# Performance work log

Hardware: AMD Instinct MI355X
Metric: run time of the kernel (lower is better)

The kernel has to match this reference:

```python
import jax, jax.numpy as jnp
import numpy as np

NUM_CODES = 1024
CODE_DIM = 64
EMA_DECAY = 0.99
COMMIT_W = 0.25
EPS = 1e-5
B = 262144


def setup_inputs() -> dict:
    key = jax.random.key(0)
    k1, k2, k3, k4 = jax.random.split(key, 4)
    z = jax.random.normal(k1, (B, CODE_DIM), dtype=jnp.float32)
    weight = jax.random.normal(k2, (NUM_CODES, CODE_DIM), dtype=jnp.float32)
    ema_cluster_size = jax.random.uniform(k3, (NUM_CODES,), dtype=jnp.float32)
    ema_embed_sum = jax.random.normal(k4, (NUM_CODES, CODE_DIM), dtype=jnp.float32)
    return {"z": z, "weight": weight, "ema_cluster_size": ema_cluster_size,
            "ema_embed_sum": ema_embed_sum}


def reference(z, weight, ema_cluster_size, ema_embed_sum):
    # Squared Euclidean distances (argmin equivalent to cdist argmin)
    # d2[b,k] = ||z_b||^2 - 2 z_b . w_k + ||w_k||^2
    z2 = jnp.sum(z * z, axis=-1, keepdims=True)          # (B, 1)
    w2 = jnp.sum(weight * weight, axis=-1)               # (K,)
    d2 = z2 - 2.0 * (z @ weight.T) + w2[None, :]         # (B, K)
    indices = jnp.argmin(d2, axis=-1)                    # (B,)
    z_q = weight[indices]                                # gather with OLD weights

    # EMA codebook update (training, ema_update=True)
    ones = jnp.ones((z.shape[0],), dtype=z.dtype)
    cluster_size = jax.ops.segment_sum(ones, indices, num_segments=NUM_CODES)
    embed_sum = jax.ops.segment_sum(z, indices, num_segments=NUM_CODES)
    new_cs = EMA_DECAY * ema_cluster_size + (1.0 - EMA_DECAY) * cluster_size
    new_es = EMA_DECAY * ema_embed_sum + (1.0 - EMA_DECAY) * embed_sum
    n = jnp.sum(new_cs)
    smoothed = (new_cs + EPS) / (n + NUM_CODES * EPS) * n
    new_weight = new_es / smoothed[:, None]

    # commitment loss (z detached in torch; pure value here)
    vq_loss = COMMIT_W * jnp.mean((z - z_q) ** 2)

    # straight-through estimator
    z_q_st = z + jax.lax.stop_gradient(z_q - z)
    return z_q_st, indices, vq_loss, new_cs, new_es, new_weight
```

## Files before the change

### kernel.cpp

```cpp
#include <hip/hip_runtime.h>

typedef __attribute__((ext_vector_type(8))) short bf16x8;
typedef __attribute__((ext_vector_type(4))) float f32x4;

#define B_ROWS 262144
#define K_CODES 1024
#define DIM 64
#define DELTA 0.015f

#define OUT_ZQ 0
#define OUT_IDX 16777216
#define OUT_LOSS 17039360
#define OUT_NEWCS 17039361
#define OUT_NEWES 17040385
#define OUT_NEWW 17105921

#define WS_LOSS   0
#define WS_QCOUNT 1
#define WS_W2     16
#define WS_SMOOTH 1040
#define WS_WHIP   2064
#define WS_WLOP   34832
#define WS_CPART  67600
#define WS_EPART  100368
#define WS_MINI   2197520
#define WS_QUEUE  2459664

static __device__ __forceinline__ unsigned short f2bf(float x) {
    unsigned u = __float_as_uint(x);
    return (unsigned short)((u + 0x7fffu + ((u >> 16) & 1u)) >> 16);
}
static __device__ __forceinline__ float bf2f(unsigned short u) {
    return __uint_as_float(((unsigned)u) << 16);
}

static __device__ __forceinline__ void cvt_frag(const float* zrow, bf16x8& hi, bf16x8& lo) {
    float4 f0 = *(const float4*)zrow;
    float4 f1 = *(const float4*)(zrow + 4);
    float tf[8] = {f0.x, f0.y, f0.z, f0.w, f1.x, f1.y, f1.z, f1.w};
#pragma unroll
    for (int j = 0; j < 8; ++j) {
        unsigned short h = f2bf(tf[j]);
        hi[j] = (short)h;
        lo[j] = (short)f2bf(tf[j] - bf2f(h));
    }
}

__global__ __launch_bounds__(256) void vq_prep(const float* __restrict__ w,
                                               float* __restrict__ ws) {
    int b = blockIdx.x, tid = threadIdx.x;
    if (b < 4) {
        int k = b * 256 + tid;
        const float4* w4 = (const float4*)(w + (size_t)k * DIM);
        float s = 0.f;
#pragma unroll
        for (int j = 0; j < 16; ++j) {
            float4 v = w4[j];
            s += v.x * v.x + v.y * v.y + v.z * v.z + v.w * v.w;
        }
        ws[WS_W2 + k] = s;
    } else {
        int i = (b - 4) * 256 + tid;
        int p = i & 1023, c = i >> 10;
        int code = c * 128 + ((p >> 7) << 4) + (p & 15);
        int octet = ((p >> 6) & 1) * 4 + ((p >> 4) & 3);
        const float* src = w + (size_t)code * DIM + octet * 8;
        float4 f0 = *(const float4*)src;
        float4 f1 = *(const float4*)(src + 4);
        float tf[8] = {f0.x, f0.y, f0.z, f0.w, f1.x, f1.y, f1.z, f1.w};
        bf16x8 hv, lv;
#pragma unroll
        for (int j = 0; j < 8; ++j) {
            unsigned short hb = f2bf(tf[j]);
            hv[j] = (short)hb;
            lv[j] = (short)f2bf(tf[j] - bf2f(hb));
        }
        ((bf16x8*)(ws + WS_WHIP))[i] = hv;
        ((bf16x8*)(ws + WS_WLOP))[i] = lv;
    }
}

__global__ __launch_bounds__(256, 2) void vq_screen_kernel(
    const float* __restrict__ z, float* __restrict__ ws) {
    __shared__ __align__(16) unsigned short lds_h[1024 * 8];
    __shared__ __align__(16) unsigned short lds_l[1024 * 8];
    __shared__ float lds_w2[K_CODES];

    int tid = threadIdx.x;
    int l = tid & 63, wave = tid >> 6;
    int m = l & 15, q = l >> 4;

    *(float4*)&lds_w2[tid * 4] = ((const float4*)(ws + WS_W2))[tid];

    int rowbase = blockIdx.x * 256 + wave * 64;
    bf16x8 ahi[4][2], alo[4][2];
#pragma unroll
    for (int g = 0; g < 4; ++g) {
        const float* zr = z + (size_t)(rowbase + g * 16 + m) * DIM + q * 8;
        cvt_frag(zr, ahi[g][0], alo[g][0]);
        cvt_frag(zr + 32, ahi[g][1], alo[g][1]);
    }

    float mv[16], m2[16];
    int mi[16];
#pragma unroll
    for (int v = 0; v < 16; ++v) { mv[v] = 3.4e38f; m2[v] = 3.4e38f; mi[v] = 0; }

    const uint4* gh = (const uint4*)(ws + WS_WHIP);
    const uint4* gl = (const uint4*)(ws + WS_WLOP);

    for (int cch = 0; cch < 8; ++cch) {
        __syncthreads();
        {
            uint4 t0 = gh[cch * 1024 + 0 * 256 + tid];
            uint4 t1 = gh[cch * 1024 + 1 * 256 + tid];
            uint4 t2 = gh[cch * 1024 + 2 * 256 + tid];
            uint4 t3 = gh[cch * 1024 + 3 * 256 + tid];
            *(uint4*)&lds_h[(unsigned)(0 * 256 + tid) * 8] = t0;
            *(uint4*)&lds_h[(unsigned)(1 * 256 + tid) * 8] = t1;
            *(uint4*)&lds_h[(unsigned)(2 * 256 + tid) * 8] = t2;
            *(uint4*)&lds_h[(unsigned)(3 * 256 + tid) * 8] = t3;
        }
        {
            uint4 t0 = gl[cch * 1024 + 0 * 256 + tid];
            uint4 t1 = gl[cch * 1024 + 1 * 256 + tid];
            uint4 t2 = gl[cch * 1024 + 2 * 256 + tid];
            uint4 t3 = gl[cch * 1024 + 3 * 256 + tid];
            *(uint4*)&lds_l[(unsigned)(0 * 256 + tid) * 8] = t0;
            *(uint4*)&lds_l[(unsigned)(1 * 256 + tid) * 8] = t1;
            *(uint4*)&lds_l[(unsigned)(2 * 256 + tid) * 8] = t2;
            *(uint4*)&lds_l[(unsigned)(3 * 256 + tid) * 8] = t3;
        }
        __syncthreads();

#pragma unroll 2
        for (int tg = 0; tg < 8; ++tg) {
            bf16x8 bh0 = *(const bf16x8*)&lds_h[(unsigned)(tg * 128 + l) * 8];
            bf16x8 bh1 = *(const bf16x8*)&lds_h[(unsigned)(tg * 128 + 64 + l) * 8];
            bf16x8 bl0 = *(const bf16x8*)&lds_l[(unsigned)(tg * 128 + l) * 8];
            bf16x8 bl1 = *(const bf16x8*)&lds_l[(unsigned)(tg * 128 + 64 + l) * 8];
            int cg = cch * 128 + tg * 16 + m;
            float w2v = lds_w2[cg];
#pragma unroll
            for (int g = 0; g < 4; ++g) {
                f32x4 acc = {0.f, 0.f, 0.f, 0.f};
                acc = __builtin_amdgcn_mfma_f32_16x16x32_bf16(alo[g][0], bh0, acc, 0, 0, 0);
                acc = __builtin_amdgcn_mfma_f32_16x16x32_bf16(ahi[g][0], bl0, acc, 0, 0, 0);
                acc = __builtin_amdgcn_mfma_f32_16x16x32_bf16(alo[g][1], bh1, acc, 0, 0, 0);
                acc = __builtin_amdgcn_mfma_f32_16x16x32_bf16(ahi[g][1], bl1, acc, 0, 0, 0);
                acc = __builtin_amdgcn_mfma_f32_16x16x32_bf16(ahi[g][0], bh0, acc, 0, 0, 0);
                acc = __builtin_amdgcn_mfma_f32_16x16x32_bf16(ahi[g][1], bh1, acc, 0, 0, 0);
#pragma unroll
                for (int r = 0; r < 4; ++r) {
                    int v = g * 4 + r;
                    float d = fmaf(acc[r], -2.0f, w2v);
                    bool lt = d < mv[v];
                    m2[v] = lt ? mv[v] : fminf(m2[v], d);
                    mv[v] = lt ? d : mv[v];
                    mi[v] = lt ? cg : mi[v];
                }
            }
        }
    }

#pragma unroll
    for (int o = 1; o < 16; o <<= 1) {
#pragma unroll
        for (int v = 0; v < 16; ++v) {
            float ov = __shfl_xor(mv[v], o, 64);
            float ov2 = __shfl_xor(m2[v], o, 64);
            int oi = __shfl_xor(mi[v], o, 64);
            float nm2 = fminf(fminf(m2[v], ov2), fmaxf(mv[v], ov));
            bool take = (ov < mv[v]) || (ov == mv[v] && oi < mi[v]);
            mv[v] = take ? ov : mv[v];
            mi[v] = take ? oi : mi[v];
            m2[v] = nm2;
        }
    }
    if (m == 0) {
#pragma unroll
        for (int v = 0; v < 16; ++v) {
            int g = v >> 2, r = v & 3;
            int row = rowbase + g * 16 + q * 4 + r;
            bool amb = (m2[v] - mv[v] <= DELTA);
            ((int*)ws)[WS_MINI + row] = mi[v] | (amb ? 0x80000000 : 0);
        }
    }
}

__global__ __launch_bounds__(256) void vq_gather_kernel(
    const float* __restrict__ z, const float* __restrict__ w,
    float* __restrict__ ws, float* __restrict__ out) {
    __shared__ float lred[4];
    int tid = threadIdx.x;
    int lane = tid & 63, wave = tid >> 6;
    int rsub = lane >> 4;
    int d4 = lane & 15;
    int wavebase = blockIdx.x * 256 + wave * 64;

    int encv[16];
#pragma unroll
    for (int s = 0; s < 16; ++s)
        encv[s] = ((const int*)ws)[WS_MINI + wavebase + s * 4 + rsub];

    float lsum = 0.f;
#pragma unroll
    for (int s = 0; s < 16; ++s) {
        int row = wavebase + s * 4 + rsub;
        int enc = encv[s];
        if (enc >= 0) {
            float4 x = ((const float4*)(z + (size_t)row * DIM))[d4];
            float4 qv = ((const float4*)(w + (size_t)enc * DIM))[d4];
            float4 st;
            st.x = x.x + (qv.x - x.x);
            st.y = x.y + (qv.y - x.y);
            st.z = x.z + (qv.z - x.z);
            st.w = x.w + (qv.w - x.w);
            ((float4*)(out + OUT_ZQ + (size_t)row * DIM))[d4] = st;
            float e0 = x.x - qv.x, e1 = x.y - qv.y, e2 = x.z - qv.z, e3 = x.w - qv.w;
            lsum += e0 * e0;
            lsum += e1 * e1;
            lsum += e2 * e2;
            lsum += e3 * e3;
            if (d4 == 0) out[OUT_IDX + row] = (float)enc;
        } else if (d4 == 0) {
            int pos = atomicAdd((int*)ws + WS_QCOUNT, 1);
            ((int*)ws)[WS_QUEUE + pos] = row;
        }
    }
#pragma unroll
    for (int o = 32; o; o >>= 1) lsum += __shfl_down(lsum, o, 64);
    if (lane == 0) lred[wave] = lsum;
    __syncthreads();
    if (tid == 0) atomicAdd(ws + WS_LOSS, lred[0] + lred[1] + lred[2] + lred[3]);
}

__global__ __launch_bounds__(256) void vq_fixup_kernel(
    const float* __restrict__ z, const float* __restrict__ w,
    float* __restrict__ ws, float* __restrict__ out) {
    const float* __restrict__ w2 = ws + WS_W2;
    int count = ((const int*)ws)[WS_QCOUNT];
    int lane = threadIdx.x & 63;
    int wv = (blockIdx.x * 256 + threadIdx.x) >> 6;
    int nw = (gridDim.x * 256) >> 6;
    for (int qi = wv; qi < count; qi += nw) {
        int row = ((const int*)ws)[WS_QUEUE + qi];
        const float* zr = z + (size_t)row * DIM;
        float zloc[DIM];
#pragma unroll
        for (int d = 0; d < DIM; ++d) zloc[d] = zr[d];
        float z2 = 0.f;
#pragma unroll
        for (int d = 0; d < DIM; ++d) z2 = fmaf(zloc[d], zloc[d], z2);
        float best = 3.4e38f;
        int bi = 0;
        for (int i = 0; i < 16; ++i) {
            int c = i * 64 + lane;
            const float* wr = w + (size_t)c * DIM;
            float a = 0.f;
#pragma unroll
            for (int d = 0; d < DIM; ++d) a = fmaf(zloc[d], wr[d], a);
            float dd = (z2 - 2.f * a) + w2[c];
            if (dd < best) { best = dd; bi = c; }
        }
#pragma unroll
        for (int o = 1; o < 64; o <<= 1) {
            float ov = __shfl_xor(best, o, 64);
            int oi = __shfl_xor(bi, o, 64);
            if (ov < best || (ov == best && oi < bi)) { best = ov; bi = oi; }
        }
        float x = zr[lane];
        float qv = w[(size_t)bi * DIM + lane];
        out[OUT_ZQ + (size_t)row * DIM + lane] = x + (qv - x);
        float e = x - qv;
        float s = e * e;
#pragma unroll
        for (int o = 32; o; o >>= 1) s += __shfl_down(s, o, 64);
        if (lane == 0) {
            out[OUT_IDX + row] = (float)bi;
            atomicAdd(ws + WS_LOSS, s);
        }
    }
}

__global__ __launch_bounds__(1024) void vq_embed_kernel(
    const float* __restrict__ z, const float* __restrict__ idx_f,
    float* __restrict__ ws) {
    __shared__ float eacc[128 * DIM];
    __shared__ float ecnt[128];
    __shared__ int lists[16][256];
    int b = blockIdx.x;
    int cs = b & 7, rs = b >> 3;
    float lo = (float)(cs * 128), hi = lo + 128.f;
    int tid = threadIdx.x;
    int wave = tid >> 6, lane = tid & 63;

#pragma unroll
    for (int j = 0; j < 8; ++j) eacc[j * 1024 + tid] = 0.f;
    if (tid < 128) ecnt[tid] = 0.f;
    __syncthreads();

    const float4* idx4 = (const float4*)idx_f;
    unsigned long long lanebits = (1ull << lane) - 1ull;
    for (int it = 0; it < 2; ++it) {
        int base = rs * 8192 + wave * 512 + it * 256;
        float4 f = idx4[(base >> 2) + lane];
        int cnt = 0;
#pragma unroll
        for (int c = 0; c < 4; ++c) {
            float fv = (c == 0) ? f.x : (c == 1) ? f.y : (c == 2) ? f.z : f.w;
            bool match = (fv >= lo && fv < hi);
            unsigned long long mmask = __ballot(match);
            if (match) {
                int pos = cnt + __popcll(mmask & lanebits);
                int row = base + 4 * lane + c;
                int local = (int)fv - cs * 128;
                lists[wave][pos] = (row << 7) | local;
                atomicAdd(&ecnt[local], 1.f);
            }
            cnt += __popcll(mmask);
        }
        int j = 0;
        for (; j + 4 <= cnt; j += 4) {
            int e0 = lists[wave][j], e1 = lists[wave][j + 1];
            int e2 = lists[wave][j + 2], e3 = lists[wave][j + 3];
            float v0 = z[(size_t)(e0 >> 7) * DIM + lane];
            float v1 = z[(size_t)(e1 >> 7) * DIM + lane];
            float v2 = z[(size_t)(e2 >> 7) * DIM + lane];
            float v3 = z[(size_t)(e3 >> 7) * DIM + lane];
            atomicAdd(&eacc[(e0 & 127) * DIM + lane], v0);
            atomicAdd(&eacc[(e1 & 127) * DIM + lane], v1);
            atomicAdd(&eacc[(e2 & 127) * DIM + lane], v2);
            atomicAdd(&eacc[(e3 & 127) * DIM + lane], v3);
        }
        for (; j < cnt; ++j) {
            int e = lists[wave][j];
            float v = z[(size_t)(e >> 7) * DIM + lane];
            atomicAdd(&eacc[(e & 127) * DIM + lane], v);
        }
    }
    __syncthreads();
#pragma unroll
    for (int j = 0; j < 8; ++j)
        ws[WS_EPART + (size_t)b * 8192 + j * 1024 + tid] = eacc[j * 1024 + tid];
    if (tid < 128) ws[WS_CPART + b * 128 + tid] = ecnt[tid];
}

__global__ __launch_bounds__(1024) void vq_finalize1_kernel(
    const float* __restrict__ ema_cs, float* __restrict__ ws,
    float* __restrict__ out) {
    int k = threadIdx.x;
    int cs = k >> 7, local = k & 127;
    float c = 0.f;
#pragma unroll
    for (int rs = 0; rs < 32; ++rs) c += ws[WS_CPART + (rs * 8 + cs) * 128 + local];
    float nc = 0.99f * ema_cs[k] + 0.01f * c;
    out[OUT_NEWCS + k] = nc;

    float s = nc;
#pragma unroll
    for (int o = 32; o; o >>= 1) s += __shfl_down(s, o, 64);
    __shared__ float red[16];
    __shared__ float n_sh;
    if ((k & 63) == 0) red[k >> 6] = s;
    __syncthreads();
    if (k == 0) {
        float n = 0.f;
#pragma unroll
        for (int i = 0; i < 16; ++i) n += red[i];
        n_sh = n;
        out[OUT_LOSS] = 0.25f * (ws[WS_LOSS] / 16777216.0f);
    }
    __syncthreads();
    float n = n_sh;
    ws[WS_SMOOTH + k] = (nc + 1e-5f) / (n + 0.01024f) * n;
}

__global__ __launch_bounds__(256) void vq_finalize2_kernel(
    const float* __restrict__ ema_es, const float* __restrict__ ws,
    float* __restrict__ out) {
    int i = blockIdx.x * 256 + threadIdx.x;
    int code = i >> 6, dim = i & 63;
    int cs = code >> 7, local = code & 127;
    float e = 0.f;
#pragma unroll
    for (int rs = 0; rs < 32; ++rs)
        e += ws[WS_EPART + (size_t)(rs * 8 + cs) * 8192 + local * DIM + dim];
    float es = 0.99f * ema_es[i] + 0.01f * e;
    out[OUT_NEWES + i] = es;
    out[OUT_NEWW + i] = es / ws[WS_SMOOTH + code];
}

extern "C" void kernel_launch(void* const* d_in, const int* in_sizes, int n_in,
                              void* d_out, int out_size, void* d_ws, size_t ws_size,
                              hipStream_t stream) {
    const float* z = (const float*)d_in[0];
    const float* weight = (const float*)d_in[1];
    const float* ema_cs = (const float*)d_in[2];
    const float* ema_es = (const float*)d_in[3];
    float* out = (float*)d_out;
    float* ws = (float*)d_ws;

    hipMemsetAsync(ws, 0, 64, stream);
    vq_prep<<<36, 256, 0, stream>>>(weight, ws);
    vq_screen_kernel<<<B_ROWS / 256, 256, 0, stream>>>(z, ws);
    vq_gather_kernel<<<B_ROWS / 256, 256, 0, stream>>>(z, weight, ws, out);
    vq_fixup_kernel<<<256, 256, 0, stream>>>(z, weight, ws, out);
    vq_embed_kernel<<<256, 1024, 0, stream>>>(z, out + OUT_IDX, ws);
    vq_finalize1_kernel<<<1, 1024, 0, stream>>>(ema_cs, ws, out);
    vq_finalize2_kernel<<<256, 256, 0, stream>>>(ema_es, ws, out);
}
```

Baseline: 414.5 us.

## Load codebook fragments directly from global memory instead of staging through LDS

Removes the per-chunk cooperative copy of the hi/lo bf16 codebook into shared memory and its two barriers per chunk. Each wave now reads its MFMA B fragments straight from global memory, relying on L1/L2 caching since every block reads the same 256KB. The top-2 min tracking is also rewritten with fminf/fmaxf to cut select instructions. The risk is that global load latency is exposed inside the MFMA loop, and the per-block LDS savings may not buy usable occupancy under the launch bounds.

```diff
diff --git a/kernel.cpp b/kernel.cpp
--- a/kernel.cpp
+++ b/kernel.cpp
@@ -82,8 +82,6 @@
 
 __global__ __launch_bounds__(256, 2) void vq_screen_kernel(
     const float* __restrict__ z, float* __restrict__ ws) {
-    __shared__ __align__(16) unsigned short lds_h[1024 * 8];
-    __shared__ __align__(16) unsigned short lds_l[1024 * 8];
     __shared__ float lds_w2[K_CODES];
 
     int tid = threadIdx.x;
@@ -106,39 +104,19 @@
 #pragma unroll
     for (int v = 0; v < 16; ++v) { mv[v] = 3.4e38f; m2[v] = 3.4e38f; mi[v] = 0; }
 
-    const uint4* gh = (const uint4*)(ws + WS_WHIP);
-    const uint4* gl = (const uint4*)(ws + WS_WLOP);
+    const bf16x8* __restrict__ gh = (const bf16x8*)(ws + WS_WHIP);
+    const bf16x8* __restrict__ gl = (const bf16x8*)(ws + WS_WLOP);
+
+    __syncthreads();
 
     for (int cch = 0; cch < 8; ++cch) {
-        __syncthreads();
-        {
-            uint4 t0 = gh[cch * 1024 + 0 * 256 + tid];
-            uint4 t1 = gh[cch * 1024 + 1 * 256 + tid];
-            uint4 t2 = gh[cch * 1024 + 2 * 256 + tid];
-            uint4 t3 = gh[cch * 1024 + 3 * 256 + tid];
-            *(uint4*)&lds_h[(unsigned)(0 * 256 + tid) * 8] = t0;
-            *(uint4*)&lds_h[(unsigned)(1 * 256 + tid) * 8] = t1;
-            *(uint4*)&lds_h[(unsigned)(2 * 256 + tid) * 8] = t2;
-            *(uint4*)&lds_h[(unsigned)(3 * 256 + tid) * 8] = t3;
-        }
-        {
-            uint4 t0 = gl[cch * 1024 + 0 * 256 + tid];
-            uint4 t1 = gl[cch * 1024 + 1 * 256 + tid];
-            uint4 t2 = gl[cch * 1024 + 2 * 256 + tid];
-            uint4 t3 = gl[cch * 1024 + 3 * 256 + tid];
-            *(uint4*)&lds_l[(unsigned)(0 * 256 + tid) * 8] = t0;
-            *(uint4*)&lds_l[(unsigned)(1 * 256 + tid) * 8] = t1;
-            *(uint4*)&lds_l[(unsigned)(2 * 256 + tid) * 8] = t2;
-            *(uint4*)&lds_l[(unsigned)(3 * 256 + tid) * 8] = t3;
-        }
-        __syncthreads();
-
 #pragma unroll 2
         for (int tg = 0; tg < 8; ++tg) {
-            bf16x8 bh0 = *(const bf16x8*)&lds_h[(unsigned)(tg * 128 + l) * 8];
-            bf16x8 bh1 = *(const bf16x8*)&lds_h[(unsigned)(tg * 128 + 64 + l) * 8];
-            bf16x8 bl0 = *(const bf16x8*)&lds_l[(unsigned)(tg * 128 + l) * 8];
-            bf16x8 bl1 = *(const bf16x8*)&lds_l[(unsigned)(tg * 128 + 64 + l) * 8];
+            int gi = cch * 1024 + tg * 128 + l;
+            bf16x8 bh0 = gh[gi];
+            bf16x8 bh1 = gh[gi + 64];
+            bf16x8 bl0 = gl[gi];
+            bf16x8 bl1 = gl[gi + 64];
             int cg = cch * 128 + tg * 16 + m;
             float w2v = lds_w2[cg];
 #pragma unroll
@@ -154,9 +132,9 @@
                 for (int r = 0; r < 4; ++r) {
                     int v = g * 4 + r;
                     float d = fmaf(acc[r], -2.0f, w2v);
+                    m2[v] = fminf(m2[v], fmaxf(mv[v], d));
                     bool lt = d < mv[v];
-                    m2[v] = lt ? mv[v] : fminf(m2[v], d);
-                    mv[v] = lt ? d : mv[v];
+                    mv[v] = fminf(mv[v], d);
                     mi[v] = lt ? cg : mi[v];
                 }
             }
```

After: 426.0 us. 2.8% more time.
